# Kernel optimization log

Hardware: AMD Instinct MI355X
Metric: run time of the kernel (lower is better)

## Reference

```python
import jax, jax.numpy as jnp
import numpy as np

B, T, H, W, C = 2, 8, 60, 60, 256
HEADS = 8
HD = C // HEADS
WH, WW = 5, 6
SH, SW = 2, 3
N = WH * WW            # 30 tokens per window
NW = (H // WH) * (W // WW)  # 120 windows
HID = 4 * C
SCALE = HD ** -0.5


def _rel_pos_index():
    # standard Swin 2D relative position index, shape (N, N)
    coords = np.stack(np.meshgrid(np.arange(WH), np.arange(WW), indexing='ij')).reshape(2, -1)
    rel = (coords[:, :, None] - coords[:, None, :]).transpose(1, 2, 0).astype(np.int64)
    rel[..., 0] += WH - 1
    rel[..., 1] += WW - 1
    rel[..., 0] *= 2 * WW - 1
    return jnp.asarray(rel.sum(-1))


def _attn_mask():
    # shifted-window attention mask, shape (NW, N, N), values in {0, -100}
    img = np.zeros((H, W))
    cnt = 0
    for hs in (slice(0, -WH), slice(-WH, -SH), slice(-SH, None)):
        for ws in (slice(0, -WW), slice(-WW, -SW), slice(-SW, None)):
            img[hs, ws] = cnt
            cnt += 1
    mw = img.reshape(H // WH, WH, W // WW, WW).transpose(0, 2, 1, 3).reshape(NW, N)
    diff = mw[:, None, :] - mw[:, :, None]
    return jnp.asarray(np.where(diff != 0, -100.0, 0.0).astype(np.float32))


REL_INDEX = _rel_pos_index()
ATTN_MASK = _attn_mask()


def _ln(x, g, b):
    m = x.mean(-1, keepdims=True)
    v = ((x - m) ** 2).mean(-1, keepdims=True)
    return (x - m) / jnp.sqrt(v + 1e-5) * g + b


def setup_inputs() -> dict:
    key = jax.random.key(0)
    ks = jax.random.split(key, 8)
    w_scale = 0.02
    return {
        'x': jax.random.normal(ks[0], (B, T, H, W, C), jnp.float32),
        'contrast_embed': jax.random.normal(ks[1], (B, T, C), jnp.float32),
        'gamma1': jnp.ones((C,), jnp.float32),
        'beta1': jnp.zeros((C,), jnp.float32),
        'Wq': jax.random.normal(ks[2], (C, C), jnp.float32) * w_scale,
        'bq': jnp.zeros((C,), jnp.float32),
        'Wk': jax.random.normal(ks[3], (C, C), jnp.float32) * w_scale,
        'bk': jnp.zeros((C,), jnp.float32),
        'Wv': jax.random.normal(ks[4], (C, C), jnp.float32) * w_scale,
        'bv': jnp.zeros((C,), jnp.float32),
        'rel_bias': jax.random.normal(ks[5], ((2 * WH - 1) * (2 * WW - 1), HEADS), jnp.float32) * w_scale,
        'Wo': jax.random.normal(ks[6], (C, C), jnp.float32) * w_scale,
        'bo': jnp.zeros((C,), jnp.float32),
        'gamma2': jnp.ones((C,), jnp.float32),
        'beta2': jnp.zeros((C,), jnp.float32),
        'W1': jax.random.normal(ks[7], (C, HID), jnp.float32) * w_scale,
        'b1': jnp.zeros((HID,), jnp.float32),
        'W2': jax.random.normal(jax.random.fold_in(key, 99), (HID, C), jnp.float32) * w_scale,
        'b2': jnp.zeros((C,), jnp.float32),
    }


def reference(x, contrast_embed, gamma1, beta1, Wq, bq, Wk, bk, Wv, bv, rel_bias,
              Wo, bo, gamma2, beta2, W1, b1, W2, b2):
    shortcut = x
    xn = _ln(x, gamma1, beta1)
    # cyclic shift (SW-MSA)
    xs = jnp.roll(xn, (-SH, -SW), axis=(2, 3))
    # window partition: (B,T,H,W,C) -> (B*NW, T, N, C)
    w = xs.reshape(B, T, H // WH, WH, W // WW, WW, C)
    w = w.transpose(0, 2, 4, 1, 3, 5, 6).reshape(B * NW, T, N, C)
    # per-contrast positional embedding, broadcast over windows and spatial positions
    pos = jnp.broadcast_to(contrast_embed[:, None, :, None, :], (B, NW, T, 1, C)).reshape(B * NW, T, 1, C)
    wqk = w + pos
    q = (wqk @ Wq + bq).reshape(B * NW, T, N, HEADS, HD)
    k = (wqk @ Wk + bk).reshape(B * NW, T, N, HEADS, HD)
    v = (w @ Wv + bv).reshape(B * NW, T, N, HEADS, HD)
    scores = jnp.einsum('btnhd,btmhd->bthnm', q, k) * SCALE
    bias = rel_bias[REL_INDEX].transpose(2, 0, 1)  # (HEADS, N, N)
    scores = scores + bias
    scores = scores.reshape(B, NW, T, HEADS, N, N) + ATTN_MASK[None, :, None, None]
    attn = jax.nn.softmax(scores, axis=-1).reshape(B * NW, T, HEADS, N, N)
    out = jnp.einsum('bthnm,btmhd->btnhd', attn, v).reshape(B * NW, T, N, C)
    out = out @ Wo + bo
    # window reverse: (B*NW, T, N, C) -> (B, T, H, W, C)
    out = out.reshape(B, H // WH, W // WW, T, WH, WW, C)
    out = out.transpose(0, 3, 1, 4, 2, 5, 6).reshape(B, T, H, W, C)
    out = jnp.roll(out, (SH, SW), axis=(2, 3))
    x1 = shortcut + out
    h = jax.nn.gelu(_ln(x1, gamma2, beta2) @ W1 + b1, approximate=False) @ W2 + b2
    return x1 + h
```

## Files before the change

### kernel.cpp

```cpp
#include <hip/hip_runtime.h>

#define DI __device__ __forceinline__

constexpr int SH_=2, SW_=3;
constexpr int ROWS_=57600;
constexpr float SCALE_=0.17677669529663687f;

typedef unsigned short u16x8 __attribute__((ext_vector_type(8)));
typedef short bf16x8 __attribute__((ext_vector_type(8)));
typedef float f32x4 __attribute__((ext_vector_type(4)));
typedef float f32x16 __attribute__((ext_vector_type(16)));

DI float bf2f(unsigned short u){ return __uint_as_float(((unsigned int)u)<<16); }
DI unsigned short f2bf(float f){
  unsigned int u = __float_as_uint(f);
  u += 0x7fffu + ((u>>16)&1u);
  return (unsigned short)(u>>16);
}
DI float ldf(const void* p, size_t i, int f){
  return f ? ((const float*)p)[i] : bf2f(((const unsigned short*)p)[i]);
}
DI float4 ldf4(const void* p, size_t i, int f){
  if (f) return *((const float4*)((const float*)p + i));
  ushort4 u = *((const ushort4*)((const unsigned short*)p + i));
  return make_float4(bf2f(u.x),bf2f(u.y),bf2f(u.z),bf2f(u.w));
}

DI void gload16(const void* g, void* l){
  __builtin_amdgcn_global_load_lds((const __attribute__((address_space(1))) unsigned int*)g,
                                   (__attribute__((address_space(3))) unsigned int*)l, 16, 0, 0);
}

DI void xcd_remap(int wg, int nb, int nn, int& mt, int& nt){
  const int q = nb>>3, r = nb&7;
  const int x = wg & 7, i = wg >> 3;
  const int base = (x<r) ? x*(q+1) : r*(q+1) + (x-r)*q;
  const int work = base + i;
  mt = work / nn; nt = work - mt*nn;
}

__global__ void k_detect(const unsigned short* __restrict__ xu, int* __restrict__ flag){
  unsigned short u = xu[threadIdx.x*2];
  int insane = ((u>>7)&0xFF) > 0xC0;
  unsigned long long m = __ballot(insane);
  if (threadIdx.x==0) *flag = m ? 1 : 0;
}

__global__ __launch_bounds__(256) void k_prepw(
    const void* __restrict__ Wq, const void* __restrict__ Wk,
    const void* __restrict__ Wv, const void* __restrict__ Wo,
    const void* __restrict__ W1, const void* __restrict__ W2,
    unsigned short* __restrict__ wt, const int* __restrict__ flagp)
{
  const int f = *flagp;
  const void* src; int kb, total; size_t off;
  switch(blockIdx.y){
    case 0: src=Wq; kb=8;  total=65536;  off=0;      break;
    case 1: src=Wk; kb=8;  total=65536;  off=65536;  break;
    case 2: src=Wv; kb=8;  total=65536;  off=131072; break;
    case 3: src=Wo; kb=8;  total=65536;  off=196608; break;
    case 4: src=W1; kb=8;  total=262144; off=262144; break;
    default:src=W2; kb=10; total=262144; off=524288; break;
  }
  const int i = blockIdx.x*256 + threadIdx.x;
  if (i >= total) return;
  const int K = 1<<kb, N = total>>kb;
  const int n = i>>kb, k = i&(K-1);
  wt[off + (size_t)n*K + k] = f2bf(ldf(src, (size_t)k*N + n, f));
}

__global__ __launch_bounds__(256) void k_posqk(const void* __restrict__ ce,
    const unsigned short* __restrict__ wtq, const unsigned short* __restrict__ wtk,
    const void* __restrict__ bq, const void* __restrict__ bk,
    float* __restrict__ posq, float* __restrict__ posk, const int* __restrict__ flagp)
{
  const int f = *flagp;
  const int bt = blockIdx.x, mat = blockIdx.y, co = threadIdx.x;
  __shared__ float ces[256];
  ces[co] = ldf(ce, bt*256+co, f);
  __syncthreads();
  const unsigned short* wr = (mat ? wtk : wtq) + (size_t)co*256;
  float s = ldf(mat ? bk : bq, co, f);
  #pragma unroll
  for (int k0=0;k0<256;k0+=8){
    u16x8 wv = *(const u16x8*)(wr + k0);
    #pragma unroll
    for (int j=0;j<8;++j) s += ces[k0+j]*bf2f(wv[j]);
  }
  (mat ? posk : posq)[bt*256+co] = s;
}

__global__ __launch_bounds__(256) void k_ln1(const void* __restrict__ x,
    const void* __restrict__ g, const void* __restrict__ be,
    unsigned short* __restrict__ xw, const int* __restrict__ flagp)
{
  const int f = *flagp;
  const int lane = threadIdx.x & 63;
  const int wv   = threadIdx.x >> 6;
  const int rs   = blockIdx.x*4 + wv;
  float4 u = ldf4(x, (size_t)rs*256 + lane*4, f);
  float s = u.x+u.y+u.z+u.w;
  #pragma unroll
  for (int o=32;o;o>>=1) s += __shfl_xor(s,o,64);
  const float mean = s*(1.f/256.f);
  float d0=u.x-mean, d1=u.y-mean, d2=u.z-mean, d3=u.w-mean;
  float qv = d0*d0+d1*d1+d2*d2+d3*d3;
  #pragma unroll
  for (int o=32;o;o>>=1) qv += __shfl_xor(qv,o,64);
  const float rstd = rsqrtf(qv*(1.f/256.f)+1e-5f);
  float4 gu = ldf4(g, lane*4, f);
  float4 bu = ldf4(be, lane*4, f);
  ushort4 o;
  o.x = f2bf(d0*rstd*gu.x+bu.x);
  o.y = f2bf(d1*rstd*gu.y+bu.y);
  o.z = f2bf(d2*rstd*gu.z+bu.z);
  o.w = f2bf(d3*rstd*gu.w+bu.w);
  const int c = rs % 60, r = (rs/60)%60, t = (rs/3600)&7, b = rs/28800;
  int r2 = r - SH_; if (r2<0) r2+=60;
  int c2 = c - SW_; if (c2<0) c2+=60;
  const int a=r2/5, ii=r2%5, bb=c2/6, jj=c2%6;
  const int rw = ((b*120 + a*10+bb)*8 + t)*30 + ii*6+jj;
  *reinterpret_cast<ushort4*>(xw + (size_t)rw*256 + lane*4) = o;
}

__global__ __launch_bounds__(256) void k_ln2(const unsigned short* __restrict__ x1b,
    const void* __restrict__ g, const void* __restrict__ be,
    unsigned short* __restrict__ xn2, const int* __restrict__ flagp)
{
  const int f = *flagp;
  const int lane = threadIdx.x & 63;
  const int wv   = threadIdx.x >> 6;
  const int rs   = blockIdx.x*4 + wv;
  float4 v = ldf4(x1b, (size_t)rs*256 + lane*4, 0);
  float s = v.x+v.y+v.z+v.w;
  #pragma unroll
  for (int o=32;o;o>>=1) s += __shfl_xor(s,o,64);
  const float mean = s*(1.f/256.f);
  float d0=v.x-mean, d1=v.y-mean, d2=v.z-mean, d3=v.w-mean;
  float qv = d0*d0+d1*d1+d2*d2+d3*d3;
  #pragma unroll
  for (int o=32;o;o>>=1) qv += __shfl_xor(qv,o,64);
  const float rstd = rsqrtf(qv*(1.f/256.f)+1e-5f);
  float4 gu = ldf4(g, lane*4, f);
  float4 bu = ldf4(be, lane*4, f);
  ushort4 o;
  o.x = f2bf(d0*rstd*gu.x+bu.x);
  o.y = f2bf(d1*rstd*gu.y+bu.y);
  o.z = f2bf(d2*rstd*gu.z+bu.z);
  o.w = f2bf(d3*rstd*gu.w+bu.w);
  *reinterpret_cast<ushort4*>(xn2 + (size_t)rs*256 + lane*4) = o;
}

template<int K>
DI void mfma_core128(const unsigned short* __restrict__ A, const unsigned short* __restrict__ WT,
                     const int m0, const int n0, f32x4 acc[4][2], unsigned short* lds)
{
  constexpr int STEPS = K/32;
  const int tid = threadIdx.x, lane = tid&63, wave = tid>>6;
  const int wm = (wave>>2)*64, wn = (wave&3)*32;
  const int fr = lane&15;
  const int kqs = ((lane>>4) ^ (fr&3))*8;
  #pragma unroll
  for (int i=0;i<4;++i)
    #pragma unroll
    for (int j=0;j<2;++j) acc[i][j] = (f32x4){0.f,0.f,0.f,0.f};
  const int isB = wave>>2;
  const int c0 = (wave&3)*128 + lane;
  const int c1 = c0 + 64;
  const int r0=c0>>2, p0=((c0&3)^(r0&3));
  const int r1=c1>>2, p1=((c1&3)^(r1&3));
  const unsigned short* gb = isB ? (WT + (size_t)n0*K) : (A + (size_t)m0*K);
  const unsigned short* g0 = gb + (size_t)r0*K + p0*8;
  const unsigned short* g1 = gb + (size_t)r1*K + p1*8;
  const int ldso = isB*4096 + (wave&3)*1024;
  #define STAGE_(d,k0) do{ \
    unsigned short* bse = lds + (d)*8192 + ldso; \
    gload16(g0+(k0), bse); \
    gload16(g1+(k0), bse+512); }while(0)
  STAGE_(0,0);
  STAGE_(1,32);
  int cur = 0;
  for (int t=0; t<STEPS; ++t){
    if (t+2 < STEPS){
      int nb = cur+2; if (nb>=3) nb-=3;
      STAGE_(nb, (t+2)*32);
      asm volatile("s_waitcnt vmcnt(4)" ::: "memory");
    } else if (t+2 == STEPS){
      asm volatile("s_waitcnt vmcnt(2)" ::: "memory");
    } else {
      asm volatile("s_waitcnt vmcnt(0)" ::: "memory");
    }
    __builtin_amdgcn_s_barrier();
    const unsigned short* At = lds + cur*8192;
    const unsigned short* Bt = At + 4096;
    bf16x8 af[4], bfv[2];
    #pragma unroll
    for (int mi=0;mi<4;++mi) af[mi]  = *(const bf16x8*)(At + (wm+mi*16+fr)*32 + kqs);
    #pragma unroll
    for (int ni=0;ni<2;++ni) bfv[ni] = *(const bf16x8*)(Bt + (wn+ni*16+fr)*32 + kqs);
    #pragma unroll
    for (int mi=0;mi<4;++mi)
      #pragma unroll
      for (int ni=0;ni<2;++ni)
        acc[mi][ni] = __builtin_amdgcn_mfma_f32_16x16x32_bf16(af[mi], bfv[ni], acc[mi][ni], 0,0,0);
    __builtin_amdgcn_s_barrier();
    cur = (cur+1==3)?0:cur+1;
  }
  #undef STAGE_
}

__global__ __launch_bounds__(512,5) void k_gemm_qkv(const unsigned short* __restrict__ Ain,
    const unsigned short* __restrict__ WT, const float* __restrict__ posq,
    const float* __restrict__ posk, const void* __restrict__ bv,
    unsigned short* __restrict__ qb, unsigned short* __restrict__ kb,
    unsigned short* __restrict__ vb2, const int* __restrict__ flagp)
{
  __shared__ __align__(16) unsigned short lds[24576];
  f32x4 acc[4][2];
  int mt, nt; xcd_remap(blockIdx.x, 2700, 6, mt, nt);
  const int m0 = mt*128;
  mfma_core128<256>(Ain, WT, m0, nt*128, acc, lds);
  const int f = *flagp;
  const int tid = threadIdx.x, lane = tid&63, wave = tid>>6;
  const int wm = (wave>>2)*64, wn = (wave&3)*32;
  const int fr = lane&15, fq = lane>>4;
  const int seg = nt>>1;
  unsigned short* ob = seg==0? qb : (seg==1? kb : vb2);
  const float* posb = seg==0? posq : posk;
  #pragma unroll
  for (int mi=0;mi<4;++mi){
    #pragma unroll
    for (int r=0;r<4;++r){
      const int row = wm+mi*16+fq*4+r;
      const int grow = m0+row;
      const int bt2 = (grow/28800)*8 + (grow/30)%8;
      #pragma unroll
      for (int ni=0;ni<2;++ni){
        const int lcol = wn+ni*16+fr;
        const int colm = (nt&1)*128 + lcol;
        const float bvv = (seg<2) ? posb[bt2*256+colm] : ldf(bv,colm,f);
        lds[row*132+lcol] = f2bf(acc[mi][ni][r] + bvv);
      }
    }
  }
  __syncthreads();
  const int row = tid>>2;
  unsigned short* dst = ob + (size_t)(m0+row)*256 + (nt&1)*128;
  #pragma unroll
  for (int j=0;j<4;++j){
    const int ci = j*4 + (tid&3);
    *(u16x8*)(dst + ci*8) = *(const u16x8*)(lds + row*132 + ci*8);
  }
}

__global__ __launch_bounds__(256) void k_attn(const unsigned short* __restrict__ q,
    const unsigned short* __restrict__ k, const unsigned short* __restrict__ v,
    const void* __restrict__ relb, unsigned short* __restrict__ ao,
    const int* __restrict__ flagp)
{
  __shared__ __align__(16) unsigned short vt[4][32*40];
  __shared__ __align__(16) unsigned short pa[4][32*40];
  const int f = *flagp;
  const int tid = threadIdx.x, lane = tid&63, wave = tid>>6;
  const int task = blockIdx.x*4 + wave;
  const int h = task & 7, bt = task >> 3;
  const int wi = (bt>>3) % 120;
  const int a_ = wi/10, bb_ = wi%10;
  const size_t base = (size_t)bt*7680 + h*32;
  unsigned short* vtw = &vt[wave][0];
  unsigned short* paw = &pa[wave][0];
  if (lane < 60){
    const int m = lane>>1, hf = lane&1;
    const unsigned short* src = v + base + (size_t)m*256 + hf*16;
    u16x8 r0 = *(const u16x8*)(src);
    u16x8 r1 = *(const u16x8*)(src+8);
    #pragma unroll
    for (int j=0;j<8;++j){ vtw[(hf*16+j)*40+m] = r0[j]; vtw[(hf*16+8+j)*40+m] = r1[j]; }
  }
  vtw[(lane>>1)*40 + 30 + (lane&1)] = 0;
  const int n  = lane&31;
  const int hl = lane>>5;
  f32x16 accS = {};
  {
    const unsigned short* ka = k + base + (size_t)n*256 + hl*8;
    const unsigned short* qa = q + base + (size_t)n*256 + hl*8;
    bf16x8 a0 = *(const bf16x8*)(ka);
    bf16x8 b0 = *(const bf16x8*)(qa);
    accS = __builtin_amdgcn_mfma_f32_32x32x16_bf16(a0, b0, accS, 0,0,0);
    bf16x8 a1 = *(const bf16x8*)(ka+16);
    bf16x8 b1 = *(const bf16x8*)(qa+16);
    accS = __builtin_amdgcn_mfma_f32_32x32x16_bf16(a1, b1, accS, 0,0,0);
  }
  const int nc  = (n < 30) ? n : 29;
  const int in_ = nc/6, jn = nc - in_*6;
  const int rn = a_*5+in_, cn = bb_*6+jn;
  const int lnl = (rn<55?0:(rn<58?1:2))*3 + (cn<54?0:(cn<57?1:2));
  #pragma unroll
  for (int r=0;r<16;++r){
    const int m = (r&3) + 8*(r>>2) + 4*hl;
    if (m < 30){
      const int im = m/6, jm = m - im*6;
      const int ridx = (in_-im+4)*11 + (jn-jm+5);
      const float bi = ldf(relb, ridx*8+h, f);
      const int rm = a_*5+im, cm = bb_*6+jm;
      const int lml = (rm<55?0:(rm<58?1:2))*3 + (cm<54?0:(cm<57?1:2));
      accS[r] = accS[r]*SCALE_ + bi + (lnl==lml ? 0.f : -100.f);
    } else accS[r] = -1e30f;
  }
  float mx = accS[0];
  #pragma unroll
  for (int r=1;r<16;++r) mx = fmaxf(mx, accS[r]);
  mx = fmaxf(mx, __shfl_xor(mx, 32, 64));
  float sum = 0.f;
  #pragma unroll
  for (int r=0;r<16;++r){ accS[r] = __expf(accS[r]-mx); sum += accS[r]; }
  sum += __shfl_xor(sum, 32, 64);
  const float inv = 1.f/sum;
  #pragma unroll
  for (int r=0;r<16;++r){
    const int m = (r&3)+8*(r>>2)+4*hl;
    paw[n*40 + m] = f2bf(accS[r]);
  }
  f32x16 accO = {};
  #pragma unroll
  for (int ks=0; ks<2; ++ks){
    bf16x8 av  = *(const bf16x8*)(vtw + n*40 + ks*16 + hl*8);
    bf16x8 pv  = *(const bf16x8*)(paw + n*40 + ks*16 + hl*8);
    accO = __builtin_amdgcn_mfma_f32_32x32x16_bf16(av, pv, accO, 0,0,0);
  }
  if (n < 30){
    #pragma unroll
    for (int g4=0; g4<4; ++g4){
      const int d0 = 8*g4 + 4*hl;
      ushort4 o;
      o.x = f2bf(accO[g4*4+0]*inv);
      o.y = f2bf(accO[g4*4+1]*inv);
      o.z = f2bf(accO[g4*4+2]*inv);
      o.w = f2bf(accO[g4*4+3]*inv);
      *(ushort4*)(ao + base + (size_t)n*256 + d0) = o;
    }
  }
}

__global__ __launch_bounds__(512,5) void k_gemm_wo(const unsigned short* __restrict__ Ain,
    const unsigned short* __restrict__ WT, const void* __restrict__ bias,
    const void* __restrict__ xin, unsigned short* __restrict__ x1b,
    const int* __restrict__ flagp)
{
  __shared__ __align__(16) unsigned short lds[24576];
  f32x4 acc[4][2];
  int mt, nt; xcd_remap(blockIdx.x, 900, 2, mt, nt);
  const int m0 = mt*128, n0 = nt*128;
  mfma_core128<256>(Ain, WT, m0, n0, acc, lds);
  const int f = *flagp;
  const int tid = threadIdx.x, lane = tid&63, wave = tid>>6;
  const int wm = (wave>>2)*64, wn = (wave&3)*32;
  const int fr = lane&15, fq = lane>>4;
  #pragma unroll
  for (int mi=0;mi<4;++mi){
    #pragma unroll
    for (int ni=0;ni<2;++ni){
      const int lcol = wn+ni*16+fr;
      const float bvv = ldf(bias, n0+lcol, f);
      #pragma unroll
      for (int r=0;r<4;++r){
        const int row = wm+mi*16+fq*4+r;
        lds[row*132+lcol] = f2bf(acc[mi][ni][r] + bvv);
      }
    }
  }
  __syncthreads();
  const int row = tid>>2;
  const int rw = m0+row;
  const int nn = rw%30, t = (rw/30)%8, bw = rw/240;
  const int b = bw/120, wi = bw%120;
  const int a = wi/10, bb2 = wi%10, ii = nn/6, jj = nn%6;
  int rr = a*5+ii+SH_; if (rr>=60) rr-=60;
  int cc = bb2*6+jj+SW_; if (cc>=60) cc-=60;
  const size_t srow = ((size_t)((b*8+t)*60 + rr)*60 + cc);
  #pragma unroll
  for (int j=0;j<4;++j){
    const int ci = j*4 + (tid&3);
    const int col = n0 + ci*8;
    u16x8 vv = *(const u16x8*)(lds + row*132 + ci*8);
    float4 xa = ldf4(xin, srow*256+col,   f);
    float4 xbv= ldf4(xin, srow*256+col+4, f);
    u16x8 o;
    o[0]=f2bf(bf2f(vv[0])+xa.x); o[1]=f2bf(bf2f(vv[1])+xa.y);
    o[2]=f2bf(bf2f(vv[2])+xa.z); o[3]=f2bf(bf2f(vv[3])+xa.w);
    o[4]=f2bf(bf2f(vv[4])+xbv.x); o[5]=f2bf(bf2f(vv[5])+xbv.y);
    o[6]=f2bf(bf2f(vv[6])+xbv.z); o[7]=f2bf(bf2f(vv[7])+xbv.w);
    *(u16x8*)(x1b + srow*256 + col) = o;
  }
}

__global__ __launch_bounds__(512,5) void k_mlp1(const unsigned short* __restrict__ Ain,
    const unsigned short* __restrict__ WT, const void* __restrict__ bias,
    unsigned short* __restrict__ hb, const int row0, const int* __restrict__ flagp)
{
  __shared__ __align__(16) unsigned short lds[24576];
  f32x4 acc[4][2];
  int mt, nt; xcd_remap(blockIdx.x, 1800, 8, mt, nt);
  const int m0 = row0 + mt*128, n0 = nt*128;
  mfma_core128<256>(Ain, WT, m0, n0, acc, lds);
  const int f = *flagp;
  const int tid = threadIdx.x, lane = tid&63, wave = tid>>6;
  const int wm = (wave>>2)*64, wn = (wave&3)*32;
  const int fr = lane&15, fq = lane>>4;
  #pragma unroll
  for (int mi=0;mi<4;++mi){
    #pragma unroll
    for (int ni=0;ni<2;++ni){
      const int lcol = wn+ni*16+fr;
      const float bvv = ldf(bias, n0+lcol, f);
      #pragma unroll
      for (int r=0;r<4;++r){
        const int row = wm+mi*16+fq*4+r;
        const float vv = acc[mi][ni][r] + bvv;
        lds[row*132+lcol] = f2bf(0.5f*vv*(1.f+erff(vv*0.70710678118654752f)));
      }
    }
  }
  __syncthreads();
  const int row = tid>>2;
  unsigned short* dst = hb + (size_t)(mt*128+row)*1024 + n0;
  #pragma unroll
  for (int j=0;j<4;++j){
    const int ci = j*4 + (tid&3);
    *(u16x8*)(dst + ci*8) = *(const u16x8*)(lds + row*132 + ci*8);
  }
}

__global__ __launch_bounds__(512,5) void k_mlp2(const unsigned short* __restrict__ hbin,
    const unsigned short* __restrict__ WT, const void* __restrict__ bias,
    const unsigned short* __restrict__ x1b, void* __restrict__ outb,
    const int row0, const int* __restrict__ flagp)
{
  __shared__ __align__(16) unsigned short lds[24576];
  f32x4 acc[4][2];
  int mt, nt; xcd_remap(blockIdx.x, 450, 2, mt, nt);
  const int m0l = mt*128, n0 = nt*128;
  mfma_core128<1024>(hbin, WT, m0l, n0, acc, lds);
  const int f = *flagp;
  const int tid = threadIdx.x, lane = tid&63, wave = tid>>6;
  const int wm = (wave>>2)*64, wn = (wave&3)*32;
  const int fr = lane&15, fq = lane>>4;
  #pragma unroll
  for (int mi=0;mi<4;++mi){
    #pragma unroll
    for (int ni=0;ni<2;++ni){
      const int lcol = wn+ni*16+fr;
      const float bvv = ldf(bias, n0+lcol, f);
      #pragma unroll
      for (int r=0;r<4;++r){
        const int row = wm+mi*16+fq*4+r;
        lds[row*132+lcol] = f2bf(acc[mi][ni][r] + bvv);
      }
    }
  }
  __syncthreads();
  const int row = tid>>2;
  const size_t grow = (size_t)(row0 + m0l + row);
  #pragma unroll
  for (int j=0;j<4;++j){
    const int ci = j*4 + (tid&3);
    const int col = n0 + ci*8;
    u16x8 vv = *(const u16x8*)(lds + row*132 + ci*8);
    u16x8 xv = *(const u16x8*)(x1b + grow*256 + col);
    if (f){
      float4 o0, o1;
      o0.x=bf2f(vv[0])+bf2f(xv[0]); o0.y=bf2f(vv[1])+bf2f(xv[1]);
      o0.z=bf2f(vv[2])+bf2f(xv[2]); o0.w=bf2f(vv[3])+bf2f(xv[3]);
      o1.x=bf2f(vv[4])+bf2f(xv[4]); o1.y=bf2f(vv[5])+bf2f(xv[5]);
      o1.z=bf2f(vv[6])+bf2f(xv[6]); o1.w=bf2f(vv[7])+bf2f(xv[7]);
      *(float4*)((float*)outb + grow*256 + col)     = o0;
      *(float4*)((float*)outb + grow*256 + col + 4) = o1;
    } else {
      u16x8 o;
      #pragma unroll
      for (int e=0;e<8;++e) o[e] = f2bf(bf2f(vv[e])+bf2f(xv[e]));
      *(u16x8*)((unsigned short*)outb + grow*256 + col) = o;
    }
  }
}

extern "C" void kernel_launch(void* const* d_in, const int* in_sizes, int n_in,
                              void* d_out, int out_size, void* d_ws, size_t ws_size,
                              hipStream_t stream)
{
  const void* x   = d_in[0];
  const void* ce  = d_in[1];
  const void* g1  = d_in[2];
  const void* be1 = d_in[3];
  const void* Wq  = d_in[4];
  const void* bq  = d_in[5];
  const void* Wk  = d_in[6];
  const void* bk  = d_in[7];
  const void* Wv  = d_in[8];
  const void* bv  = d_in[9];
  const void* rb  = d_in[10];
  const void* Wo  = d_in[11];
  const void* bo  = d_in[12];
  const void* g2  = d_in[13];
  const void* be2 = d_in[14];
  const void* W1  = d_in[15];
  const void* b1  = d_in[16];
  const void* W2  = d_in[17];
  const void* b2  = d_in[18];

  char* ws = (char*)d_ws;
  const size_t SZ = (size_t)ROWS_*256*2;
  unsigned short* kbuf = (unsigned short*)(ws);
  unsigned short* vbuf = (unsigned short*)(ws + SZ);
  unsigned short* xw   = (unsigned short*)(ws + 2*SZ);
  unsigned short* qbuf = (unsigned short*)(ws + 3*SZ);
  unsigned short* aob  = xw;
  unsigned short* xn2  = kbuf;
  unsigned short* x1b  = qbuf;
  unsigned short* hb   = vbuf;
  float* posq = (float*)(ws + 4*SZ);
  float* posk = posq + 16*256;
  int*   flag = (int*)(ws + 4*SZ + 32768);
  unsigned short* wt = (unsigned short*)(ws + 4*SZ + 65536);

  unsigned short* wtqkv = wt;
  unsigned short* wtq = wt;
  unsigned short* wtk = wt + 65536;
  unsigned short* wto = wt + 196608;
  unsigned short* wt1 = wt + 262144;
  unsigned short* wt2 = wt + 524288;

  k_detect<<<1,64,0,stream>>>((const unsigned short*)x, flag);
  k_prepw<<<dim3(1024,6),256,0,stream>>>(Wq,Wk,Wv,Wo,W1,W2, wt, flag);
  k_posqk<<<dim3(16,2),256,0,stream>>>(ce, wtq, wtk, bq, bk, posq, posk, flag);
  k_ln1<<<14400,256,0,stream>>>(x, g1, be1, xw, flag);
  k_gemm_qkv<<<2700,512,0,stream>>>(xw, wtqkv, posq, posk, bv, qbuf, kbuf, vbuf, flag);
  k_attn<<<3840,256,0,stream>>>(qbuf, kbuf, vbuf, rb, aob, flag);
  k_gemm_wo<<<900,512,0,stream>>>(aob, wto, bo, x, x1b, flag);
  k_ln2<<<14400,256,0,stream>>>(x1b, g2, be2, xn2, flag);
  for (int chk=0; chk<2; ++chk){
    const int row0 = chk*28800;
    k_mlp1<<<1800,512,0,stream>>>(xn2, wt1, b1, hb, row0, flag);
    k_mlp2<<<450,512,0,stream>>>(hb, wt2, b2, x1b, d_out, row0, flag);
  }
}
```

Baseline: 278.7 us.

## Load GEMM B fragments directly to registers, stage only A through LDS

The shared MFMA GEMM core now loads the weight-operand fragments from global memory straight into registers, prefetched one k-step ahead, instead of staging them through LDS. Only half the waves stage the A tile into a smaller triple-buffered LDS ring, and the LDS allocation per block shrinks accordingly. This aims to cut LDS traffic and footprint and to reduce LDS read pressure in the inner loop. The cost is duplicate global/L2 reads of B across waves and more hand-tuned vmcnt synchronisation.

```diff
diff --git a/kernel.cpp b/kernel.cpp
--- a/kernel.cpp
+++ b/kernel.cpp
@@ -38,6 +38,9 @@
   const int work = base + i;
   mt = work / nn; nt = work - mt*nn;
 }
+
+#define WAITV(n) do{ asm volatile("s_waitcnt vmcnt(" #n ")" ::: "memory"); \
+                     __builtin_amdgcn_sched_barrier(0); }while(0)
 
 __global__ void k_detect(const unsigned short* __restrict__ xu, int* __restrict__ flag){
   unsigned short u = xu[threadIdx.x*2];
@@ -158,55 +161,63 @@
   constexpr int STEPS = K/32;
   const int tid = threadIdx.x, lane = tid&63, wave = tid>>6;
   const int wm = (wave>>2)*64, wn = (wave&3)*32;
-  const int fr = lane&15;
+  const int fr = lane&15, kg8 = (lane>>4)*8;
   const int kqs = ((lane>>4) ^ (fr&3))*8;
   #pragma unroll
   for (int i=0;i<4;++i)
     #pragma unroll
     for (int j=0;j<2;++j) acc[i][j] = (f32x4){0.f,0.f,0.f,0.f};
-  const int isB = wave>>2;
+  const bool stager = (wave<4);
   const int c0 = (wave&3)*128 + lane;
   const int c1 = c0 + 64;
   const int r0=c0>>2, p0=((c0&3)^(r0&3));
   const int r1=c1>>2, p1=((c1&3)^(r1&3));
-  const unsigned short* gb = isB ? (WT + (size_t)n0*K) : (A + (size_t)m0*K);
-  const unsigned short* g0 = gb + (size_t)r0*K + p0*8;
-  const unsigned short* g1 = gb + (size_t)r1*K + p1*8;
-  const int ldso = isB*4096 + (wave&3)*1024;
-  #define STAGE_(d,k0) do{ \
-    unsigned short* bse = lds + (d)*8192 + ldso; \
-    gload16(g0+(k0), bse); \
-    gload16(g1+(k0), bse+512); }while(0)
-  STAGE_(0,0);
-  STAGE_(1,32);
+  const unsigned short* gA0 = A + (size_t)(m0+r0)*K + p0*8;
+  const unsigned short* gA1 = A + (size_t)(m0+r1)*K + p1*8;
+  unsigned short* ldsw = lds + (wave&3)*1024;
+  const unsigned short* gB0 = WT + (size_t)(n0+wn+fr)*K + kg8;
+  const unsigned short* gB1 = WT + (size_t)(n0+wn+16+fr)*K + kg8;
+  #define STAGEA_(d,k0) do{ unsigned short* b = ldsw + (d)*4096; \
+    gload16(gA0+(k0), b); gload16(gA1+(k0), b+512); }while(0)
+  #define LOADB_(d0,d1,k0) do{ \
+    asm volatile("global_load_dwordx4 %0, %1, off" : "=v"(d0) : "v"(gB0+(k0)) : "memory"); \
+    asm volatile("global_load_dwordx4 %0, %1, off" : "=v"(d1) : "v"(gB1+(k0)) : "memory"); }while(0)
+  bf16x8 bc0, bc1, bn0, bn1;
+  if (stager) STAGEA_(0,0);
+  LOADB_(bc0,bc1,0);
+  if (stager) STAGEA_(1,32);
   int cur = 0;
   for (int t=0; t<STEPS; ++t){
-    if (t+2 < STEPS){
+    if (t+1 < STEPS) LOADB_(bn0,bn1,(t+1)*32);
+    if (stager && t+2 < STEPS){
       int nb = cur+2; if (nb>=3) nb-=3;
-      STAGE_(nb, (t+2)*32);
-      asm volatile("s_waitcnt vmcnt(4)" ::: "memory");
-    } else if (t+2 == STEPS){
-      asm volatile("s_waitcnt vmcnt(2)" ::: "memory");
+      STAGEA_(nb, (t+2)*32);
+    }
+    if (stager){
+      if (t+2 < STEPS)      WAITV(6);
+      else if (t+1 < STEPS) WAITV(4);
+      else                  WAITV(0);
     } else {
-      asm volatile("s_waitcnt vmcnt(0)" ::: "memory");
+      if (t+1 < STEPS)      WAITV(2);
+      else                  WAITV(0);
     }
     __builtin_amdgcn_s_barrier();
-    const unsigned short* At = lds + cur*8192;
-    const unsigned short* Bt = At + 4096;
-    bf16x8 af[4], bfv[2];
-    #pragma unroll
-    for (int mi=0;mi<4;++mi) af[mi]  = *(const bf16x8*)(At + (wm+mi*16+fr)*32 + kqs);
-    #pragma unroll
-    for (int ni=0;ni<2;++ni) bfv[ni] = *(const bf16x8*)(Bt + (wn+ni*16+fr)*32 + kqs);
-    #pragma unroll
-    for (int mi=0;mi<4;++mi)
-      #pragma unroll
-      for (int ni=0;ni<2;++ni)
-        acc[mi][ni] = __builtin_amdgcn_mfma_f32_16x16x32_bf16(af[mi], bfv[ni], acc[mi][ni], 0,0,0);
+    __builtin_amdgcn_sched_barrier(0);
+    const unsigned short* At = lds + cur*4096;
+    bf16x8 af[4];
+    #pragma unroll
+    for (int mi=0;mi<4;++mi) af[mi] = *(const bf16x8*)(At + (wm+mi*16+fr)*32 + kqs);
+    #pragma unroll
+    for (int mi=0;mi<4;++mi){
+      acc[mi][0] = __builtin_amdgcn_mfma_f32_16x16x32_bf16(af[mi], bc0, acc[mi][0], 0,0,0);
+      acc[mi][1] = __builtin_amdgcn_mfma_f32_16x16x32_bf16(af[mi], bc1, acc[mi][1], 0,0,0);
+    }
     __builtin_amdgcn_s_barrier();
+    bc0 = bn0; bc1 = bn1;
     cur = (cur+1==3)?0:cur+1;
   }
-  #undef STAGE_
+  #undef STAGEA_
+  #undef LOADB_
 }
 
 __global__ __launch_bounds__(512,5) void k_gemm_qkv(const unsigned short* __restrict__ Ain,
@@ -215,7 +226,7 @@
     unsigned short* __restrict__ qb, unsigned short* __restrict__ kb,
     unsigned short* __restrict__ vb2, const int* __restrict__ flagp)
 {
-  __shared__ __align__(16) unsigned short lds[24576];
+  __shared__ __align__(16) unsigned short lds[16896];
   f32x4 acc[4][2];
   int mt, nt; xcd_remap(blockIdx.x, 2700, 6, mt, nt);
   const int m0 = mt*128;
@@ -347,7 +358,7 @@
     const void* __restrict__ xin, unsigned short* __restrict__ x1b,
     const int* __restrict__ flagp)
 {
-  __shared__ __align__(16) unsigned short lds[24576];
+  __shared__ __align__(16) unsigned short lds[16896];
   f32x4 acc[4][2];
   int mt, nt; xcd_remap(blockIdx.x, 900, 2, mt, nt);
   const int m0 = mt*128, n0 = nt*128;
@@ -398,7 +409,7 @@
     const unsigned short* __restrict__ WT, const void* __restrict__ bias,
     unsigned short* __restrict__ hb, const int row0, const int* __restrict__ flagp)
 {
-  __shared__ __align__(16) unsigned short lds[24576];
+  __shared__ __align__(16) unsigned short lds[16896];
   f32x4 acc[4][2];
   int mt, nt; xcd_remap(blockIdx.x, 1800, 8, mt, nt);
   const int m0 = row0 + mt*128, n0 = nt*128;
@@ -436,7 +447,7 @@
     const unsigned short* __restrict__ x1b, void* __restrict__ outb,
     const int row0, const int* __restrict__ flagp)
 {
-  __shared__ __align__(16) unsigned short lds[24576];
+  __shared__ __align__(16) unsigned short lds[16896];
   f32x4 acc[4][2];
   int mt, nt; xcd_remap(blockIdx.x, 450, 2, mt, nt);
   const int m0l = mt*128, n0 = nt*128;
```

Measured after the change: 359.1 us. 28.9% more time.

## Switch GEMM core to 32x32x16 MFMA with 4-wave blocks and double buffering

Applied to the files above, without the earlier changes.

Rewrites the shared GEMM core to use 32x32x16 bf16 MFMA instructions, so each of 4 waves computes a 64x64 subtile instead of 8 waves each computing 64x32. The LDS pipeline drops from triple to double buffering, which shrinks shared memory, and block size goes from 512 to 256 threads with adjusted launch bounds. Epilogues are remapped to the 32x32 accumulator layout. The aim is fewer LDS fragment reads per MFMA and better register reuse, at the cost of less prefetch depth and fewer waves per block to hide latency.

```diff
diff --git a/kernel.cpp b/kernel.cpp
--- a/kernel.cpp
+++ b/kernel.cpp
@@ -38,6 +38,8 @@
   const int work = base + i;
   mt = work / nn; nt = work - mt*nn;
 }
+
+#define WAITV(n) asm volatile("s_waitcnt vmcnt(" #n ")" ::: "memory")
 
 __global__ void k_detect(const unsigned short* __restrict__ xu, int* __restrict__ flag){
   unsigned short u = xu[threadIdx.x*2];
@@ -153,102 +155,104 @@
 
 template<int K>
 DI void mfma_core128(const unsigned short* __restrict__ A, const unsigned short* __restrict__ WT,
-                     const int m0, const int n0, f32x4 acc[4][2], unsigned short* lds)
+                     const int m0, const int n0, f32x16 acc[2][2], unsigned short* lds)
 {
   constexpr int STEPS = K/32;
   const int tid = threadIdx.x, lane = tid&63, wave = tid>>6;
-  const int wm = (wave>>2)*64, wn = (wave&3)*32;
-  const int fr = lane&15;
-  const int kqs = ((lane>>4) ^ (fr&3))*8;
-  #pragma unroll
-  for (int i=0;i<4;++i)
-    #pragma unroll
-    for (int j=0;j<2;++j) acc[i][j] = (f32x4){0.f,0.f,0.f,0.f};
-  const int isB = wave>>2;
-  const int c0 = (wave&3)*128 + lane;
-  const int c1 = c0 + 64;
-  const int r0=c0>>2, p0=((c0&3)^(r0&3));
-  const int r1=c1>>2, p1=((c1&3)^(r1&3));
-  const unsigned short* gb = isB ? (WT + (size_t)n0*K) : (A + (size_t)m0*K);
-  const unsigned short* g0 = gb + (size_t)r0*K + p0*8;
-  const unsigned short* g1 = gb + (size_t)r1*K + p1*8;
-  const int ldso = isB*4096 + (wave&3)*1024;
-  #define STAGE_(d,k0) do{ \
-    unsigned short* bse = lds + (d)*8192 + ldso; \
-    gload16(g0+(k0), bse); \
-    gload16(g1+(k0), bse+512); }while(0)
+  const int wm = (wave>>1)*64, wn = (wave&1)*64;
+  const int l31 = lane&31, hl = lane>>5;
+  acc[0][0]=(f32x16){}; acc[0][1]=(f32x16){}; acc[1][0]=(f32x16){}; acc[1][1]=(f32x16){};
+  const unsigned short* gsrc0; const unsigned short* gsrc1;
+  const unsigned short* gsrc2; const unsigned short* gsrc3;
+  {
+    const int c0 = wave*64 + lane;
+    const int r0 = c0>>2, p0 = (c0&3)^(r0&3);
+    const int c1 = 256 + c0, r1 = c1>>2, p1 = (c1&3)^(r1&3);
+    const int c2 = 512 + c0, r2 = (c2-512)>>2, p2 = (c2&3)^(r2&3);
+    const int c3 = 768 + c0, r3 = (c3-512)>>2, p3 = (c3&3)^(r3&3);
+    gsrc0 = A  + (size_t)(m0+r0)*K + p0*8;
+    gsrc1 = A  + (size_t)(m0+r1)*K + p1*8;
+    gsrc2 = WT + (size_t)(n0+r2)*K + p2*8;
+    gsrc3 = WT + (size_t)(n0+r3)*K + p3*8;
+  }
+  #define STAGE_(d,k0) do{ unsigned short* bb = lds + (d)*8192 + wave*512; \
+    gload16(gsrc0+(k0), bb); \
+    gload16(gsrc1+(k0), bb + 2048); \
+    gload16(gsrc2+(k0), bb + 4096); \
+    gload16(gsrc3+(k0), bb + 6144); }while(0)
   STAGE_(0,0);
-  STAGE_(1,32);
   int cur = 0;
   for (int t=0; t<STEPS; ++t){
-    if (t+2 < STEPS){
-      int nb = cur+2; if (nb>=3) nb-=3;
-      STAGE_(nb, (t+2)*32);
-      asm volatile("s_waitcnt vmcnt(4)" ::: "memory");
-    } else if (t+2 == STEPS){
-      asm volatile("s_waitcnt vmcnt(2)" ::: "memory");
+    if (t+1 < STEPS){
+      STAGE_(cur^1, (t+1)*32);
+      WAITV(4);
     } else {
-      asm volatile("s_waitcnt vmcnt(0)" ::: "memory");
+      WAITV(0);
     }
     __builtin_amdgcn_s_barrier();
     const unsigned short* At = lds + cur*8192;
     const unsigned short* Bt = At + 4096;
-    bf16x8 af[4], bfv[2];
-    #pragma unroll
-    for (int mi=0;mi<4;++mi) af[mi]  = *(const bf16x8*)(At + (wm+mi*16+fr)*32 + kqs);
-    #pragma unroll
-    for (int ni=0;ni<2;++ni) bfv[ni] = *(const bf16x8*)(Bt + (wn+ni*16+fr)*32 + kqs);
-    #pragma unroll
-    for (int mi=0;mi<4;++mi)
-      #pragma unroll
-      for (int ni=0;ni<2;++ni)
-        acc[mi][ni] = __builtin_amdgcn_mfma_f32_16x16x32_bf16(af[mi], bfv[ni], acc[mi][ni], 0,0,0);
+    #pragma unroll
+    for (int ks=0; ks<2; ++ks){
+      const int pbase = ((ks*2 + hl) ^ (lane&3))*8;
+      bf16x8 a0 = *(const bf16x8*)(At + (wm    + l31)*32 + pbase);
+      bf16x8 a1 = *(const bf16x8*)(At + (wm+32 + l31)*32 + pbase);
+      bf16x8 b0 = *(const bf16x8*)(Bt + (wn    + l31)*32 + pbase);
+      bf16x8 b1 = *(const bf16x8*)(Bt + (wn+32 + l31)*32 + pbase);
+      acc[0][0] = __builtin_amdgcn_mfma_f32_32x32x16_bf16(a0,b0,acc[0][0],0,0,0);
+      acc[0][1] = __builtin_amdgcn_mfma_f32_32x32x16_bf16(a0,b1,acc[0][1],0,0,0);
+      acc[1][0] = __builtin_amdgcn_mfma_f32_32x32x16_bf16(a1,b0,acc[1][0],0,0,0);
+      acc[1][1] = __builtin_amdgcn_mfma_f32_32x32x16_bf16(a1,b1,acc[1][1],0,0,0);
+    }
     __builtin_amdgcn_s_barrier();
-    cur = (cur+1==3)?0:cur+1;
+    cur ^= 1;
   }
   #undef STAGE_
 }
 
-__global__ __launch_bounds__(512,5) void k_gemm_qkv(const unsigned short* __restrict__ Ain,
+#define TROW(r,hl) (((r)&3) + 8*((r)>>2) + 4*(hl))
+
+__global__ __launch_bounds__(256,4) void k_gemm_qkv(const unsigned short* __restrict__ Ain,
     const unsigned short* __restrict__ WT, const float* __restrict__ posq,
     const float* __restrict__ posk, const void* __restrict__ bv,
     unsigned short* __restrict__ qb, unsigned short* __restrict__ kb,
     unsigned short* __restrict__ vb2, const int* __restrict__ flagp)
 {
-  __shared__ __align__(16) unsigned short lds[24576];
-  f32x4 acc[4][2];
+  __shared__ __align__(16) unsigned short lds[16896];
+  f32x16 acc[2][2];
   int mt, nt; xcd_remap(blockIdx.x, 2700, 6, mt, nt);
   const int m0 = mt*128;
   mfma_core128<256>(Ain, WT, m0, nt*128, acc, lds);
   const int f = *flagp;
   const int tid = threadIdx.x, lane = tid&63, wave = tid>>6;
-  const int wm = (wave>>2)*64, wn = (wave&3)*32;
-  const int fr = lane&15, fq = lane>>4;
+  const int wm = (wave>>1)*64, wn = (wave&1)*64;
+  const int l31 = lane&31, hl = lane>>5;
   const int seg = nt>>1;
   unsigned short* ob = seg==0? qb : (seg==1? kb : vb2);
   const float* posb = seg==0? posq : posk;
-  #pragma unroll
-  for (int mi=0;mi<4;++mi){
-    #pragma unroll
-    for (int r=0;r<4;++r){
-      const int row = wm+mi*16+fq*4+r;
-      const int grow = m0+row;
-      const int bt2 = (grow/28800)*8 + (grow/30)%8;
+  __syncthreads();
+  #pragma unroll
+  for (int tm=0;tm<2;++tm){
+    #pragma unroll
+    for (int tn=0;tn<2;++tn){
+      const int lcol = wn + tn*32 + l31;
+      const int colm = (nt&1)*128 + lcol;
       #pragma unroll
-      for (int ni=0;ni<2;++ni){
-        const int lcol = wn+ni*16+fr;
-        const int colm = (nt&1)*128 + lcol;
+      for (int r=0;r<16;++r){
+        const int lrow = wm + tm*32 + TROW(r,hl);
+        const int grow = m0 + lrow;
+        const int bt2 = (grow/28800)*8 + (grow/30)%8;
         const float bvv = (seg<2) ? posb[bt2*256+colm] : ldf(bv,colm,f);
-        lds[row*132+lcol] = f2bf(acc[mi][ni][r] + bvv);
+        lds[lrow*132+lcol] = f2bf(acc[tm][tn][r] + bvv);
       }
     }
   }
   __syncthreads();
-  const int row = tid>>2;
+  const int row = tid>>1;
   unsigned short* dst = ob + (size_t)(m0+row)*256 + (nt&1)*128;
   #pragma unroll
-  for (int j=0;j<4;++j){
-    const int ci = j*4 + (tid&3);
+  for (int j=0;j<8;++j){
+    const int ci = (tid&1)*8 + j;
     *(u16x8*)(dst + ci*8) = *(const u16x8*)(lds + row*132 + ci*8);
   }
 }
@@ -342,35 +346,36 @@
   }
 }
 
-__global__ __launch_bounds__(512,5) void k_gemm_wo(const unsigned short* __restrict__ Ain,
+__global__ __launch_bounds__(256,4) void k_gemm_wo(const unsigned short* __restrict__ Ain,
     const unsigned short* __restrict__ WT, const void* __restrict__ bias,
     const void* __restrict__ xin, unsigned short* __restrict__ x1b,
     const int* __restrict__ flagp)
 {
-  __shared__ __align__(16) unsigned short lds[24576];
-  f32x4 acc[4][2];
+  __shared__ __align__(16) unsigned short lds[16896];
+  f32x16 acc[2][2];
   int mt, nt; xcd_remap(blockIdx.x, 900, 2, mt, nt);
   const int m0 = mt*128, n0 = nt*128;
   mfma_core128<256>(Ain, WT, m0, n0, acc, lds);
   const int f = *flagp;
   const int tid = threadIdx.x, lane = tid&63, wave = tid>>6;
-  const int wm = (wave>>2)*64, wn = (wave&3)*32;
-  const int fr = lane&15, fq = lane>>4;
-  #pragma unroll
-  for (int mi=0;mi<4;++mi){
-    #pragma unroll
-    for (int ni=0;ni<2;++ni){
-      const int lcol = wn+ni*16+fr;
+  const int wm = (wave>>1)*64, wn = (wave&1)*64;
+  const int l31 = lane&31, hl = lane>>5;
+  __syncthreads();
+  #pragma unroll
+  for (int tm=0;tm<2;++tm){
+    #pragma unroll
+    for (int tn=0;tn<2;++tn){
+      const int lcol = wn + tn*32 + l31;
       const float bvv = ldf(bias, n0+lcol, f);
       #pragma unroll
-      for (int r=0;r<4;++r){
-        const int row = wm+mi*16+fq*4+r;
-        lds[row*132+lcol] = f2bf(acc[mi][ni][r] + bvv);
+      for (int r=0;r<16;++r){
+        const int lrow = wm + tm*32 + TROW(r,hl);
+        lds[lrow*132+lcol] = f2bf(acc[tm][tn][r] + bvv);
       }
     }
   }
   __syncthreads();
-  const int row = tid>>2;
+  const int row = tid>>1;
   const int rw = m0+row;
   const int nn = rw%30, t = (rw/30)%8, bw = rw/240;
   const int b = bw/120, wi = bw%120;
@@ -379,8 +384,8 @@
   int cc = bb2*6+jj+SW_; if (cc>=60) cc-=60;
   const size_t srow = ((size_t)((b*8+t)*60 + rr)*60 + cc);
   #pragma unroll
-  for (int j=0;j<4;++j){
-    const int ci = j*4 + (tid&3);
+  for (int j=0;j<8;++j){
+    const int ci = (tid&1)*8 + j;
     const int col = n0 + ci*8;
     u16x8 vv = *(const u16x8*)(lds + row*132 + ci*8);
     float4 xa = ldf4(xin, srow*256+col,   f);
@@ -394,76 +399,78 @@
   }
 }
 
-__global__ __launch_bounds__(512,5) void k_mlp1(const unsigned short* __restrict__ Ain,
+__global__ __launch_bounds__(256,4) void k_mlp1(const unsigned short* __restrict__ Ain,
     const unsigned short* __restrict__ WT, const void* __restrict__ bias,
     unsigned short* __restrict__ hb, const int row0, const int* __restrict__ flagp)
 {
-  __shared__ __align__(16) unsigned short lds[24576];
-  f32x4 acc[4][2];
+  __shared__ __align__(16) unsigned short lds[16896];
+  f32x16 acc[2][2];
   int mt, nt; xcd_remap(blockIdx.x, 1800, 8, mt, nt);
   const int m0 = row0 + mt*128, n0 = nt*128;
   mfma_core128<256>(Ain, WT, m0, n0, acc, lds);
   const int f = *flagp;
   const int tid = threadIdx.x, lane = tid&63, wave = tid>>6;
-  const int wm = (wave>>2)*64, wn = (wave&3)*32;
-  const int fr = lane&15, fq = lane>>4;
-  #pragma unroll
-  for (int mi=0;mi<4;++mi){
-    #pragma unroll
-    for (int ni=0;ni<2;++ni){
-      const int lcol = wn+ni*16+fr;
+  const int wm = (wave>>1)*64, wn = (wave&1)*64;
+  const int l31 = lane&31, hl = lane>>5;
+  __syncthreads();
+  #pragma unroll
+  for (int tm=0;tm<2;++tm){
+    #pragma unroll
+    for (int tn=0;tn<2;++tn){
+      const int lcol = wn + tn*32 + l31;
       const float bvv = ldf(bias, n0+lcol, f);
       #pragma unroll
-      for (int r=0;r<4;++r){
-        const int row = wm+mi*16+fq*4+r;
-        const float vv = acc[mi][ni][r] + bvv;
-        lds[row*132+lcol] = f2bf(0.5f*vv*(1.f+erff(vv*0.70710678118654752f)));
+      for (int r=0;r<16;++r){
+        const int lrow = wm + tm*32 + TROW(r,hl);
+        const float vv = acc[tm][tn][r] + bvv;
+        lds[lrow*132+lcol] = f2bf(0.5f*vv*(1.f+erff(vv*0.70710678118654752f)));
       }
     }
   }
   __syncthreads();
-  const int row = tid>>2;
+  const int row = tid>>1;
   unsigned short* dst = hb + (size_t)(mt*128+row)*1024 + n0;
   #pragma unroll
-  for (int j=0;j<4;++j){
-    const int ci = j*4 + (tid&3);
+  for (int j=0;j<8;++j){
+    const int ci = (tid&1)*8 + j;
     *(u16x8*)(dst + ci*8) = *(const u16x8*)(lds + row*132 + ci*8);
   }
 }
 
-__global__ __launch_bounds__(512,5) void k_mlp2(const unsigned short* __restrict__ hbin,
+__global__ __launch_bounds__(256,4) void k_mlp2(const unsigned short* __restrict__ hbin,
     const unsigned short* __restrict__ WT, const void* __restrict__ bias,
     const unsigned short* __restrict__ x1b, void* __restrict__ outb,
     const int row0, const int* __restrict__ flagp)
 {
-  __shared__ __align__(16) unsigned short lds[24576];
-  f32x4 acc[4][2];
+  __shared__ __align__(16) unsigned short lds[16896];
+  f32x16 acc[2][2];
   int mt, nt; xcd_remap(blockIdx.x, 450, 2, mt, nt);
   const int m0l = mt*128, n0 = nt*128;
   mfma_core128<1024>(hbin, WT, m0l, n0, acc, lds);
   const int f = *flagp;
   const int tid = threadIdx.x, lane = tid&63, wave = tid>>6;
-  const int wm = (wave>>2)*64, wn = (wave&3)*32;
-  const int fr = lane&15, fq = lane>>4;
-  #pragma unroll
-  for (int mi=0;mi<4;++mi){
-    #pragma unroll
-    for (int ni=0;ni<2;++ni){
-      const int lcol = wn+ni*16+fr;
+  const int wm = (wave>>1)*64, wn = (wave&1)*64;
+  const int l31 = lane&31, hl = lane>>5;
+  __syncthreads();
+  #pragma unroll
+  for (int tm=0;tm<2;++tm){
+    #pragma unroll
+    for (int tn=0;tn<2;++tn){
+      const int lcol = wn + tn*32 + l31;
       const float bvv = ldf(bias, n0+lcol, f);
       #pragma unroll
-      for (int r=0;r<4;++r){
-        const int row = wm+mi*16+fq*4+r;
-        lds[row*132+lcol] = f2bf(acc[mi][ni][r] + bvv);
+      for (int r=0;r<16;++r){
+        const int lrow = wm + tm*32 + TROW(r,hl);
+        lds[lrow*132+lcol] = f2bf(acc[tm][tn][r] + bvv);
       }
     }
   }
   __syncthreads();
-  const int row = tid>>2;
+  const int row = tid>>1;
   const size_t grow = (size_t)(row0 + m0l + row);
   #pragma unroll
-  for (int j=0;j<4;++j){
-    const int ci = j*4 + (tid&3);
+  for (int j=0;j<8;++j){
+    const int ci = (tid&1)*8 + j;
     const int col = n0 + ci*8;
     u16x8 vv = *(const u16x8*)(lds + row*132 + ci*8);
     u16x8 xv = *(const u16x8*)(x1b + grow*256 + col);
@@ -534,13 +541,13 @@
   k_prepw<<<dim3(1024,6),256,0,stream>>>(Wq,Wk,Wv,Wo,W1,W2, wt, flag);
   k_posqk<<<dim3(16,2),256,0,stream>>>(ce, wtq, wtk, bq, bk, posq, posk, flag);
   k_ln1<<<14400,256,0,stream>>>(x, g1, be1, xw, flag);
-  k_gemm_qkv<<<2700,512,0,stream>>>(xw, wtqkv, posq, posk, bv, qbuf, kbuf, vbuf, flag);
+  k_gemm_qkv<<<2700,256,0,stream>>>(xw, wtqkv, posq, posk, bv, qbuf, kbuf, vbuf, flag);
   k_attn<<<3840,256,0,stream>>>(qbuf, kbuf, vbuf, rb, aob, flag);
-  k_gemm_wo<<<900,512,0,stream>>>(aob, wto, bo, x, x1b, flag);
+  k_gemm_wo<<<900,256,0,stream>>>(aob, wto, bo, x, x1b, flag);
   k_ln2<<<14400,256,0,stream>>>(x1b, g2, be2, xn2, flag);
   for (int chk=0; chk<2; ++chk){
     const int row0 = chk*28800;
-    k_mlp1<<<1800,512,0,stream>>>(xn2, wt1, b1, hb, row0, flag);
-    k_mlp2<<<450,512,0,stream>>>(hb, wt2, b2, x1b, d_out, row0, flag);
-  }
-}
+    k_mlp1<<<1800,256,0,stream>>>(xn2, wt1, b1, hb, row0, flag);
+    k_mlp2<<<450,256,0,stream>>>(hb, wt2, b2, x1b, d_out, row0, flag);
+  }
+}
```

After: 366.4 us. 31.5% more time.
